# Performance work log

Hardware: AMD Instinct MI355X
Metric: run time of the kernel (lower is better)

The kernel has to match this reference:

```python
import jax, jax.numpy as jnp
import numpy as np

D_MODEL = 2048
NUM_HEADS = 32
NUM_GROUPS = 8
HEAD_DIM = D_MODEL // NUM_HEADS  # 64
HEADS_PER_GROUP = NUM_HEADS // NUM_GROUPS  # 4


def setup_inputs() -> dict:
    key = jax.random.key(0)
    ks = jax.random.split(key, 5)
    B, S = 1, 2048
    x = jax.random.normal(ks[0], (B, S, D_MODEL), dtype=jnp.float32)
    scale = 1.0 / np.sqrt(D_MODEL)
    w_q = jax.random.normal(ks[1], (D_MODEL, D_MODEL), dtype=jnp.float32) * scale
    w_k = jax.random.normal(ks[2], (D_MODEL, NUM_GROUPS * HEAD_DIM), dtype=jnp.float32) * scale
    w_v = jax.random.normal(ks[3], (D_MODEL, NUM_GROUPS * HEAD_DIM), dtype=jnp.float32) * scale
    w_o = jax.random.normal(ks[4], (D_MODEL, D_MODEL), dtype=jnp.float32) * scale
    return {"x": x, "w_q": w_q, "w_k": w_k, "w_v": w_v, "w_o": w_o}


def reference(x, w_q, w_k, w_v, w_o):
    B, S, _ = x.shape
    # projections (nn.Linear, no bias)
    q = (x @ w_q).reshape(B, S, NUM_HEADS, HEAD_DIM)          # [B,S,H,d]
    k = (x @ w_k).reshape(B, S, NUM_GROUPS, HEAD_DIM)         # [B,S,G,d]
    v = (x @ w_v).reshape(B, S, NUM_GROUPS, HEAD_DIM)
    # group queries: [B,S,G,hpg,d] so each KV group serves heads_per_group query heads
    qg = q.reshape(B, S, NUM_GROUPS, HEADS_PER_GROUP, HEAD_DIM)
    scale = 1.0 / jnp.sqrt(jnp.asarray(HEAD_DIM, dtype=x.dtype))
    # scores: [B,G,hpg,S_q,S_k] without duplicating K/V
    scores = jnp.einsum("bsghd,btgd->bghst", qg, k) * scale
    attn = jax.nn.softmax(scores, axis=-1)
    out = jnp.einsum("bghst,btgd->bsghd", attn, v)            # [B,S,G,hpg,d]
    out = out.reshape(B, S, D_MODEL)
    return out @ w_o
```

## Files before the change

### kernel.cpp

```cpp
#include <hip/hip_runtime.h>

typedef unsigned short ushort_t;
typedef __attribute__((ext_vector_type(8))) short short8;
typedef __attribute__((ext_vector_type(4))) float floatx4;

__device__ __forceinline__ unsigned short f2bf(float f) {
  unsigned int u = __float_as_uint(f);
  u += 0x7fffu + ((u >> 16) & 1u);
  return (unsigned short)(u >> 16);
}

__device__ __forceinline__ unsigned int cvt_pk_bf16(float a, float b) {
  unsigned int r;
  asm("v_cvt_pk_bf16_f32 %0, %1, %2" : "=v"(r) : "v"(a), "v"(b));
  return r;
}

__device__ __forceinline__ void gl_lds16(const void* g, void* l) {
  __builtin_amdgcn_global_load_lds((const __attribute__((address_space(1))) void*)g,
                                   (__attribute__((address_space(3))) void*)l,
                                   16, 0, 0);
}

__global__ __launch_bounds__(256) void prep_kernel(
    const float* __restrict__ x, const float* __restrict__ wq, const float* __restrict__ wk,
    const float* __restrict__ wv, const float* __restrict__ wo,
    ushort_t* __restrict__ xb, ushort_t* __restrict__ wqkvT, ushort_t* __restrict__ woT) {
  __shared__ float tile[32][33];
  int bid = blockIdx.x;
  const int t = threadIdx.x;
  if (bid < 4096) {
    int i = bid * 256 + t;
    float4 v = ((const float4*)x)[i];
    union { ushort_t u[4]; unsigned long long ll; } o;
    o.u[0] = f2bf(v.x); o.u[1] = f2bf(v.y); o.u[2] = f2bf(v.z); o.u[3] = f2bf(v.w);
    ((unsigned long long*)xb)[i] = o.ll;
    return;
  }
  const float* src; ushort_t* dst; int C, bx, by;
  if (bid < 8192)       { bid -= 4096;  src = wq; dst = wqkvT;              C = 2048; bx = bid & 63; by = bid >> 6; }
  else if (bid < 9216)  { bid -= 8192;  src = wk; dst = wqkvT + 2048 * 2048; C = 512;  bx = bid & 15; by = bid >> 4; }
  else if (bid < 10240) { bid -= 9216;  src = wv; dst = wqkvT + 2560 * 2048; C = 512;  bx = bid & 15; by = bid >> 4; }
  else                  { bid -= 10240; src = wo; dst = woT;                C = 2048; bx = bid & 63; by = bid >> 6; }
  const int R = 2048;
  int tx = t & 31, ty = t >> 5;
  int c0 = bx * 32, r0 = by * 32;
#pragma unroll
  for (int i = ty; i < 32; i += 8)
    tile[i][tx] = src[(long)(r0 + i) * C + c0 + tx];
  __syncthreads();
#pragma unroll
  for (int i = ty; i < 32; i += 8)
    dst[(long)(c0 + i) * R + r0 + tx] = f2bf(tile[tx][i]);
}

template <int BM, int BN, int EPI>
__global__ __launch_bounds__(256, (BM == 64 ? 4 : 3)) void gemm_bt(
    const ushort_t* __restrict__ A, const ushort_t* __restrict__ B,
    float* __restrict__ C,
    ushort_t* __restrict__ qb, ushort_t* __restrict__ kb, ushort_t* __restrict__ vb,
    int M, int N, int K) {
  constexpr int MI = BM / 32;
  constexpr int NJ = BN / 32;
  __shared__ __attribute__((aligned(16))) ushort_t As[2][BM * 32];
  __shared__ __attribute__((aligned(16))) ushort_t Bs[2][BN * 32];
  const int t = threadIdx.x;
  const int w = t >> 6, lane = t & 63;
  const int m = lane & 15, quad = lane >> 4;
  const int nwg = gridDim.x * gridDim.y;
  const int bid = blockIdx.y * gridDim.x + blockIdx.x;
  const int sw = (bid & 7) * (nwg >> 3) + (bid >> 3);
  const int m0 = (sw / gridDim.x) * BM, n0 = (sw % gridDim.x) * BN;
  const int wr = w >> 1, wc = w & 1;

  floatx4 acc[MI][NJ] = {};

  auto stage = [&](int kk, int buf) {
#pragma unroll
    for (int i = 0; i < BM / 64; ++i) {
      int c = i * 256 + t;
      gl_lds16(A + (long)(m0 + (c >> 2)) * K + kk + (c & 3) * 8,
               As[buf] + (i * 256 + w * 64) * 8);
    }
#pragma unroll
    for (int i = 0; i < BN / 64; ++i) {
      int c = i * 256 + t;
      gl_lds16(B + (long)(n0 + (c >> 2)) * K + kk + (c & 3) * 8,
               Bs[buf] + (i * 256 + w * 64) * 8);
    }
  };

  stage(0, 0);
  __syncthreads();
  int cur = 0;
  for (int kk = 0; kk < K; kk += 32) {
    if (kk + 32 < K) stage(kk + 32, cur ^ 1);
    short8 af[MI], bf[NJ];
#pragma unroll
    for (int i = 0; i < MI; ++i)
      af[i] = *(const short8*)(As[cur] + (wr * (BM / 2) + i * 16 + m) * 32 + quad * 8);
#pragma unroll
    for (int j = 0; j < NJ; ++j)
      bf[j] = *(const short8*)(Bs[cur] + (wc * (BN / 2) + j * 16 + m) * 32 + quad * 8);
#pragma unroll
    for (int i = 0; i < MI; ++i)
#pragma unroll
      for (int j = 0; j < NJ; ++j)
        acc[i][j] = __builtin_amdgcn_mfma_f32_16x16x32_bf16(af[i], bf[j], acc[i][j], 0, 0, 0);
    __syncthreads();
    cur ^= 1;
  }

#pragma unroll
  for (int i = 0; i < MI; ++i)
#pragma unroll
    for (int j = 0; j < NJ; ++j)
#pragma unroll
      for (int r = 0; r < 4; ++r) {
        float v = acc[i][j][r];
        int row = m0 + wr * (BM / 2) + i * 16 + quad * 4 + r;
        int col = n0 + wc * (BN / 2) + j * 16 + m;
        if (EPI == 1) {
          C[(long)row * N + col] = v;
        } else {
          if (col < 2048) {
            qb[((((col >> 6) * 2048) + row) << 6) | (col & 63)] = f2bf(v * 0.18033688f);
          } else if (col < 2560) {
            int g = (col - 2048) >> 6;
            kb[(((g * 2048) + row) << 6) | (col & 63)] = f2bf(v);
          } else {
            int g = (col - 2560) >> 6;
            vb[(long)((g << 6) | (col & 63)) * 2048 + row] = f2bf(v);
          }
        }
      }
}

__global__ __launch_bounds__(128, 2) void flash_kernel(
    const ushort_t* __restrict__ Q, const ushort_t* __restrict__ Kb,
    const ushort_t* __restrict__ Vb, ushort_t* __restrict__ O, int S) {
  __shared__ __attribute__((aligned(16))) ushort_t Ks[2][64 * 64];
  __shared__ __attribute__((aligned(16))) ushort_t Vs[2][64 * 64];
  __shared__ __attribute__((aligned(16))) ushort_t Ps[2 * 2 * 16 * 64];
  const int t = threadIdx.x;
  const int w = t >> 6, lane = t & 63;
  const int m = lane & 15, quad = lane >> 4;
  const int nwg = gridDim.x * gridDim.y;
  const int bid = blockIdx.y * gridDim.x + blockIdx.x;
  const int sw = (bid & 7) * (nwg >> 3) + (bid >> 3);
  const int h = sw / gridDim.x, g = h >> 2;
  const int q0 = (sw % gridDim.x) * 64;
  const ushort_t* qp = Q + (long)h * S * 64;
  const ushort_t* kp = Kb + (long)g * S * 64;
  const ushort_t* vp = Vb + (long)g * 64 * S;

  auto stage = [&](int t0, int buf) {
#pragma unroll
    for (int i = 0; i < 4; ++i) {
      int c = i * 128 + t;
      int c0 = i * 128 + w * 64;
      int sl = ((c & 3) ^ ((c >> 3) & 3)) * 8;
      gl_lds16(kp + (long)(t0 + ((c >> 2) & 63)) * 64 + (c >> 8) * 32 + sl, Ks[buf] + c0 * 8);
      gl_lds16(vp + (long)((c >> 2) & 63) * S + t0 + (c >> 8) * 32 + sl, Vs[buf] + c0 * 8);
    }
  };

  stage(0, 0);

  short8 qf[2][2];
#pragma unroll
  for (int rt = 0; rt < 2; ++rt)
#pragma unroll
    for (int kq = 0; kq < 2; ++kq)
      qf[rt][kq] = *(const short8*)(qp + (long)(q0 + w * 32 + rt * 16 + m) * 64 + kq * 32 + quad * 8);

  short8 ones;
#pragma unroll
  for (int z = 0; z < 8; ++z) ones[z] = (short)0x3F80;

  floatx4 lacc[2] = {};
  floatx4 oacc[2][4] = {};
  char* PwB = (char*)Ps + w * 4096;
  const int psw = (m & 7) << 4;
  const int kvswz = (quad ^ ((m >> 1) & 3)) * 8;

  __syncthreads();
  int cur = 0;
  for (int t0 = 0; t0 < S; t0 += 64) {
    if (t0 + 64 < S) stage(t0 + 64, cur ^ 1);

    floatx4 sacc[2][4] = {};
    __builtin_amdgcn_s_setprio(1);
#pragma unroll
    for (int ct = 0; ct < 4; ++ct) {
      short8 kf0 = *(const short8*)(Ks[cur] + (ct * 16 + m) * 32 + kvswz);
      short8 kf1 = *(const short8*)(Ks[cur] + 2048 + (ct * 16 + m) * 32 + kvswz);
#pragma unroll
      for (int rt = 0; rt < 2; ++rt) {
        sacc[rt][ct] = __builtin_amdgcn_mfma_f32_16x16x32_bf16(kf0, qf[rt][0], sacc[rt][ct], 0, 0, 0);
        sacc[rt][ct] = __builtin_amdgcn_mfma_f32_16x16x32_bf16(kf1, qf[rt][1], sacc[rt][ct], 0, 0, 0);
      }
    }
    __builtin_amdgcn_s_setprio(0);

#pragma unroll
    for (int rt = 0; rt < 2; ++rt)
#pragma unroll
      for (int ct = 0; ct < 4; ++ct) {
        float p0 = exp2f(sacc[rt][ct][0]);
        float p1 = exp2f(sacc[rt][ct][1]);
        float p2 = exp2f(sacc[rt][ct][2]);
        float p3 = exp2f(sacc[rt][ct][3]);
        uint2 pk;
        pk.x = cvt_pk_bf16(p0, p1);
        pk.y = cvt_pk_bf16(p2, p3);
        *(uint2*)(PwB + rt * 2048 + m * 128 + ((ct * 32 + quad * 8) ^ psw)) = pk;
      }

    __builtin_amdgcn_s_setprio(1);
#pragma unroll
    for (int kt = 0; kt < 2; ++kt) {
      short8 pf[2];
#pragma unroll
      for (int rt = 0; rt < 2; ++rt) {
        pf[rt] = *(const short8*)(PwB + rt * 2048 + m * 128 + ((kt * 64 + quad * 16) ^ psw));
        lacc[rt] = __builtin_amdgcn_mfma_f32_16x16x32_bf16(pf[rt], ones, lacc[rt], 0, 0, 0);
      }
#pragma unroll
      for (int ct = 0; ct < 4; ++ct) {
        short8 vf = *(const short8*)(Vs[cur] + kt * 2048 + (ct * 16 + m) * 32 + kvswz);
#pragma unroll
        for (int rt = 0; rt < 2; ++rt)
          oacc[rt][ct] = __builtin_amdgcn_mfma_f32_16x16x32_bf16(pf[rt], vf, oacc[rt][ct], 0, 0, 0);
      }
    }
    __builtin_amdgcn_s_setprio(0);

    __syncthreads();
    cur ^= 1;
  }

#pragma unroll
  for (int rt = 0; rt < 2; ++rt)
#pragma unroll
    for (int r = 0; r < 4; ++r) {
      float inv = 1.f / lacc[rt][r];
      int srow = q0 + w * 32 + rt * 16 + quad * 4 + r;
#pragma unroll
      for (int ct = 0; ct < 4; ++ct)
        O[(long)srow * 2048 + h * 64 + ct * 16 + m] = f2bf(oacc[rt][ct][r] * inv);
    }
}


extern "C" void kernel_launch(void* const* d_in, const int* in_sizes, int n_in,
                              void* d_out, int out_size, void* d_ws, size_t ws_size,
                              hipStream_t stream) {
  (void)in_sizes; (void)n_in; (void)out_size; (void)ws_size;
  const float* x  = (const float*)d_in[0];
  const float* wq = (const float*)d_in[1];
  const float* wk = (const float*)d_in[2];
  const float* wv = (const float*)d_in[3];
  const float* wo = (const float*)d_in[4];
  float* out = (float*)d_out;
  char* ws = (char*)d_ws;
  const size_t MB = 1u << 20;

  ushort_t* xb    = (ushort_t*)(ws);
  ushort_t* wqkvT = (ushort_t*)(ws + 8 * MB);
  ushort_t* woT   = (ushort_t*)(ws + 20 * MB);
  ushort_t* qbuf  = (ushort_t*)(ws + 28 * MB);
  ushort_t* kbuf  = (ushort_t*)(ws + 36 * MB);
  ushort_t* vbuf  = (ushort_t*)(ws + 38 * MB);
  ushort_t* attn  = xb;

  prep_kernel<<<14336, 256, 0, stream>>>(x, wq, wk, wv, wo, xb, wqkvT, woT);

  gemm_bt<128, 64, 0><<<dim3(48, 16), 256, 0, stream>>>(xb, wqkvT, nullptr, qbuf, kbuf, vbuf,
                                                        2048, 3072, 2048);
  flash_kernel<<<dim3(32, 32), 128, 0, stream>>>(qbuf, kbuf, vbuf, attn, 2048);
  gemm_bt<64, 64, 1><<<dim3(32, 32), 256, 0, stream>>>(attn, woT, out, nullptr, nullptr, nullptr,
                                                       2048, 2048, 2048);
}
```

Baseline: 246.7 us.

## Parameterize GEMM warp layout and widen flash attention blocks to 128 queries

```diff
diff --git a/kernel.cpp b/kernel.cpp
--- a/kernel.cpp
+++ b/kernel.cpp
@@ -38,10 +38,10 @@
     return;
   }
   const float* src; ushort_t* dst; int C, bx, by;
-  if (bid < 8192)       { bid -= 4096;  src = wq; dst = wqkvT;              C = 2048; bx = bid & 63; by = bid >> 6; }
+  if (bid < 8192)       { bid -= 4096;  src = wq; dst = wqkvT;               C = 2048; bx = bid & 63; by = bid >> 6; }
   else if (bid < 9216)  { bid -= 8192;  src = wk; dst = wqkvT + 2048 * 2048; C = 512;  bx = bid & 15; by = bid >> 4; }
   else if (bid < 10240) { bid -= 9216;  src = wv; dst = wqkvT + 2560 * 2048; C = 512;  bx = bid & 15; by = bid >> 4; }
-  else                  { bid -= 10240; src = wo; dst = woT;                C = 2048; bx = bid & 63; by = bid >> 6; }
+  else                  { bid -= 10240; src = wo; dst = woT;                 C = 2048; bx = bid & 63; by = bid >> 6; }
   const int R = 2048;
   int tx = t & 31, ty = t >> 5;
   int c0 = bx * 32, r0 = by * 32;
@@ -54,14 +54,15 @@
     dst[(long)(c0 + i) * R + r0 + tx] = f2bf(tile[tx][i]);
 }
 
-template <int BM, int BN, int EPI>
-__global__ __launch_bounds__(256, (BM == 64 ? 4 : 3)) void gemm_bt(
+template <int BM, int BN, int WM, int WN, int EPI>
+__global__ __launch_bounds__(WM * WN * 64, 2) void gemm_bt(
     const ushort_t* __restrict__ A, const ushort_t* __restrict__ B,
     float* __restrict__ C,
     ushort_t* __restrict__ qb, ushort_t* __restrict__ kb, ushort_t* __restrict__ vb,
     int M, int N, int K) {
-  constexpr int MI = BM / 32;
-  constexpr int NJ = BN / 32;
+  constexpr int T = WM * WN * 64;
+  constexpr int MI = BM / WM / 16;
+  constexpr int NJ = BN / WN / 16;
   __shared__ __attribute__((aligned(16))) ushort_t As[2][BM * 32];
   __shared__ __attribute__((aligned(16))) ushort_t Bs[2][BN * 32];
   const int t = threadIdx.x;
@@ -71,22 +72,20 @@
   const int bid = blockIdx.y * gridDim.x + blockIdx.x;
   const int sw = (bid & 7) * (nwg >> 3) + (bid >> 3);
   const int m0 = (sw / gridDim.x) * BM, n0 = (sw % gridDim.x) * BN;
-  const int wr = w >> 1, wc = w & 1;
+  const int wr = w / WN, wc = w % WN;
 
   floatx4 acc[MI][NJ] = {};
 
   auto stage = [&](int kk, int buf) {
 #pragma unroll
-    for (int i = 0; i < BM / 64; ++i) {
-      int c = i * 256 + t;
-      gl_lds16(A + (long)(m0 + (c >> 2)) * K + kk + (c & 3) * 8,
-               As[buf] + (i * 256 + w * 64) * 8);
-    }
-#pragma unroll
-    for (int i = 0; i < BN / 64; ++i) {
-      int c = i * 256 + t;
-      gl_lds16(B + (long)(n0 + (c >> 2)) * K + kk + (c & 3) * 8,
-               Bs[buf] + (i * 256 + w * 64) * 8);
+    for (int i = 0; i < BM * 4 / T; ++i) {
+      int c = i * T + t;
+      gl_lds16(A + (long)(m0 + (c >> 2)) * K + kk + (c & 3) * 8, As[buf] + c * 8);
+    }
+#pragma unroll
+    for (int i = 0; i < BN * 4 / T; ++i) {
+      int c = i * T + t;
+      gl_lds16(B + (long)(n0 + (c >> 2)) * K + kk + (c & 3) * 8, Bs[buf] + c * 8);
     }
   };
 
@@ -98,10 +97,10 @@
     short8 af[MI], bf[NJ];
 #pragma unroll
     for (int i = 0; i < MI; ++i)
-      af[i] = *(const short8*)(As[cur] + (wr * (BM / 2) + i * 16 + m) * 32 + quad * 8);
+      af[i] = *(const short8*)(As[cur] + (wr * (BM / WM) + i * 16 + m) * 32 + quad * 8);
 #pragma unroll
     for (int j = 0; j < NJ; ++j)
-      bf[j] = *(const short8*)(Bs[cur] + (wc * (BN / 2) + j * 16 + m) * 32 + quad * 8);
+      bf[j] = *(const short8*)(Bs[cur] + (wc * (BN / WN) + j * 16 + m) * 32 + quad * 8);
 #pragma unroll
     for (int i = 0; i < MI; ++i)
 #pragma unroll
@@ -118,8 +117,8 @@
 #pragma unroll
       for (int r = 0; r < 4; ++r) {
         float v = acc[i][j][r];
-        int row = m0 + wr * (BM / 2) + i * 16 + quad * 4 + r;
-        int col = n0 + wc * (BN / 2) + j * 16 + m;
+        int row = m0 + wr * (BM / WM) + i * 16 + quad * 4 + r;
+        int col = n0 + wc * (BN / WN) + j * 16 + m;
         if (EPI == 1) {
           C[(long)row * N + col] = v;
         } else {
@@ -136,12 +135,12 @@
       }
 }
 
-__global__ __launch_bounds__(128, 2) void flash_kernel(
+__global__ __launch_bounds__(256, 2) void flash_kernel(
     const ushort_t* __restrict__ Q, const ushort_t* __restrict__ Kb,
     const ushort_t* __restrict__ Vb, ushort_t* __restrict__ O, int S) {
   __shared__ __attribute__((aligned(16))) ushort_t Ks[2][64 * 64];
   __shared__ __attribute__((aligned(16))) ushort_t Vs[2][64 * 64];
-  __shared__ __attribute__((aligned(16))) ushort_t Ps[2 * 2 * 16 * 64];
+  __shared__ __attribute__((aligned(16))) ushort_t Ps[4 * 2 * 16 * 64];
   const int t = threadIdx.x;
   const int w = t >> 6, lane = t & 63;
   const int m = lane & 15, quad = lane >> 4;
@@ -149,16 +148,16 @@
   const int bid = blockIdx.y * gridDim.x + blockIdx.x;
   const int sw = (bid & 7) * (nwg >> 3) + (bid >> 3);
   const int h = sw / gridDim.x, g = h >> 2;
-  const int q0 = (sw % gridDim.x) * 64;
+  const int q0 = (sw % gridDim.x) * 128;
   const ushort_t* qp = Q + (long)h * S * 64;
   const ushort_t* kp = Kb + (long)g * S * 64;
   const ushort_t* vp = Vb + (long)g * 64 * S;
 
   auto stage = [&](int t0, int buf) {
 #pragma unroll
-    for (int i = 0; i < 4; ++i) {
-      int c = i * 128 + t;
-      int c0 = i * 128 + w * 64;
+    for (int i = 0; i < 2; ++i) {
+      int c = i * 256 + t;
+      int c0 = i * 256 + w * 64;
       int sl = ((c & 3) ^ ((c >> 3) & 3)) * 8;
       gl_lds16(kp + (long)(t0 + ((c >> 2) & 63)) * 64 + (c >> 8) * 32 + sl, Ks[buf] + c0 * 8);
       gl_lds16(vp + (long)((c >> 2) & 63) * S + t0 + (c >> 8) * 32 + sl, Vs[buf] + c0 * 8);
@@ -276,9 +275,9 @@
 
   prep_kernel<<<14336, 256, 0, stream>>>(x, wq, wk, wv, wo, xb, wqkvT, woT);
 
-  gemm_bt<128, 64, 0><<<dim3(48, 16), 256, 0, stream>>>(xb, wqkvT, nullptr, qbuf, kbuf, vbuf,
-                                                        2048, 3072, 2048);
-  flash_kernel<<<dim3(32, 32), 128, 0, stream>>>(qbuf, kbuf, vbuf, attn, 2048);
-  gemm_bt<64, 64, 1><<<dim3(32, 32), 256, 0, stream>>>(attn, woT, out, nullptr, nullptr, nullptr,
-                                                       2048, 2048, 2048);
-}
+  gemm_bt<128, 64, 2, 1, 0><<<dim3(48, 16), 128, 0, stream>>>(xb, wqkvT, nullptr, qbuf, kbuf, vbuf,
+                                                              2048, 3072, 2048);
+  flash_kernel<<<dim3(16, 32), 256, 0, stream>>>(qbuf, kbuf, vbuf, attn, 2048);
+  gemm_bt<64, 64, 2, 2, 1><<<dim3(32, 32), 256, 0, stream>>>(attn, woT, out, nullptr, nullptr, nullptr,
+                                                             2048, 2048, 2048);
+}
```

New measurement: 242.0 us. No clear change (-1.9%).
